# Kernel tuning notes

Measured on AMD Instinct MI355X. Metric: run time of the kernel, lower is better.

The kernel has to match this reference:

```python
import jax, jax.numpy as jnp
import numpy as np
import math

B, T, C, H = 2, 1024, 768, 12
HD = C // H


def _heads(t):
    # [B,T,C] -> [B,H,T,HD]
    return t.reshape(B, T, H, HD).transpose(0, 2, 1, 3)


def _causal_sdpa(q, k, v):
    # q,k,v: [B,H,T,HD]; scaled dot-product attention with causal mask, no dropout
    scale = 1.0 / math.sqrt(HD)
    s = jnp.einsum('bhqd,bhkd->bhqk', q, k) * scale
    mask = jnp.tril(jnp.ones((T, T), dtype=bool))
    s = jnp.where(mask, s, jnp.finfo(s.dtype).min)
    p = jax.nn.softmax(s, axis=-1)
    return jnp.einsum('bhqk,bhkd->bhqd', p, v)


def setup_inputs() -> dict:
    key = jax.random.key(0)
    k1, k2, k3 = jax.random.split(key, 3)
    x = jax.random.normal(k1, (B, T, C), dtype=jnp.float32)
    eps = 0.1
    x_lower = x - eps
    x_upper = x + eps
    W_attn = jax.random.normal(k2, (3 * C, C), dtype=jnp.float32) * 0.02
    W_proj = jax.random.normal(k3, (C, C), dtype=jnp.float32) * 0.02
    return {'x': x, 'x_lower': x_lower, 'x_upper': x_upper,
            'W_attn': W_attn, 'W_proj': W_proj}


def reference(x, x_lower, x_upper, W_attn, W_proj):
    # main path
    qkv = x @ W_attn.T                       # [B,T,3C]
    q, k, v = jnp.split(qkv, 3, axis=2)
    y = _causal_sdpa(_heads(q), _heads(k), _heads(v))
    y = y.transpose(0, 2, 1, 3).reshape(B, T, C) @ W_proj.T

    # interval bound path (torch runs it under no_grad)
    W_pos = jnp.maximum(W_attn, 0.0)
    W_neg = jnp.minimum(W_attn, 0.0)
    lowers = x_lower @ W_pos.T + x_upper @ W_neg.T   # lower bounds of q,k,v concat
    uppers = x_upper @ W_pos.T + x_lower @ W_neg.T   # upper bounds of q,k,v concat
    qL, kL, vL = (_heads(t) for t in jnp.split(lowers, 3, axis=2))
    qU, kU, vU = (_heads(t) for t in jnp.split(uppers, 3, axis=2))

    y_min = None
    y_max = None
    for qq in (qL, qU):
        for kk in (kL, kU):
            for vv in (vL, vU):
                yb = _causal_sdpa(qq, kk, vv)
                y_min = yb if y_min is None else jnp.minimum(y_min, yb)
                y_max = yb if y_max is None else jnp.maximum(y_max, yb)
    y_lower = y_min.transpose(0, 2, 1, 3).reshape(B, T, C) @ W_proj.T
    y_upper = y_max.transpose(0, 2, 1, 3).reshape(B, T, C) @ W_proj.T
    return (y, y_lower, y_upper)
```

## Files before the change

kernel.cpp:

```cpp
#include <hip/hip_runtime.h>
#include <stdint.h>
#include <math.h>

typedef __attribute__((ext_vector_type(8))) short bf16x8;
typedef __attribute__((ext_vector_type(4))) short s16x4;
typedef __attribute__((ext_vector_type(8))) short s16x8;
typedef __attribute__((ext_vector_type(4))) float f32x4;
typedef __attribute__((ext_vector_type(2))) uint32_t u32x2;

#define DEVI __device__ __forceinline__

constexpr int Bn = 2, Tn = 1024, Cn = 768, Hn = 12, HDn = 64;
constexpr int N3 = 3 * Cn;
constexpr int Mrows = Bn * Tn;
constexpr size_t SZy = (size_t)Mrows * Cn;

template <int V> struct IntC { static constexpr int value = V; };

DEVI short f2bf(float f) {
  union { float f; uint32_t u; } v; v.f = f;
  uint32_t u = v.u;
  return (short)((u + 0x7FFFu + ((u >> 16) & 1u)) >> 16);
}
DEVI float bf2f(short b) {
  union { uint32_t u; float f; } v; v.u = ((uint32_t)(uint16_t)b) << 16;
  return v.f;
}
DEVI float fexp2(float x) { return __builtin_exp2f(x); }
DEVI uint32_t cvtpk(float lo, float hi) {
  uint32_t r;
  asm("v_cvt_pk_bf16_f32 %0, %1, %2" : "=v"(r) : "v"(lo), "v"(hi));
  return r;
}
DEVI void cp16(void* lds, const void* g) {
  __builtin_amdgcn_global_load_lds(
      (const __attribute__((address_space(1))) uint32_t*)(uintptr_t)g,
      (__attribute__((address_space(3))) uint32_t*)(uint32_t)(uintptr_t)lds,
      16, 0, 0);
}
DEVI f32x4 fz() { f32x4 z; z[0] = 0.f; z[1] = 0.f; z[2] = 0.f; z[3] = 0.f; return z; }

__global__ void prep_x(const float* __restrict__ x, const float* __restrict__ xl,
                       const float* __restrict__ xu, short* __restrict__ xb,
                       short* __restrict__ mb, short* __restrict__ rb) {
  int i = blockIdx.x * 256 + threadIdx.x;
  float4 vx = ((const float4*)x)[i];
  float4 vl = ((const float4*)xl)[i];
  float4 vu = ((const float4*)xu)[i];
  s16x4 a, m_, g;
  a[0] = f2bf(vx.x); a[1] = f2bf(vx.y); a[2] = f2bf(vx.z); a[3] = f2bf(vx.w);
  m_[0] = f2bf(0.5f * (vl.x + vu.x)); m_[1] = f2bf(0.5f * (vl.y + vu.y));
  m_[2] = f2bf(0.5f * (vl.z + vu.z)); m_[3] = f2bf(0.5f * (vl.w + vu.w));
  g[0] = f2bf(0.5f * (vu.x - vl.x)); g[1] = f2bf(0.5f * (vu.y - vl.y));
  g[2] = f2bf(0.5f * (vu.z - vl.z)); g[3] = f2bf(0.5f * (vu.w - vl.w));
  ((s16x4*)xb)[i] = a; ((s16x4*)mb)[i] = m_; ((s16x4*)rb)[i] = g;
}
__global__ void prep_w(const float* __restrict__ w, short* __restrict__ wb,
                       short* __restrict__ awb) {
  int i = blockIdx.x * 256 + threadIdx.x;
  float4 v = ((const float4*)w)[i];
  s16x4 a, b2;
  a[0] = f2bf(v.x); a[1] = f2bf(v.y); a[2] = f2bf(v.z); a[3] = f2bf(v.w);
  b2[0] = f2bf(fabsf(v.x)); b2[1] = f2bf(fabsf(v.y));
  b2[2] = f2bf(fabsf(v.z)); b2[3] = f2bf(fabsf(v.w));
  ((s16x4*)wb)[i] = a; ((s16x4*)awb)[i] = b2;
}
__global__ void prep_w1(const float* __restrict__ w, short* __restrict__ wb) {
  int i = blockIdx.x * 256 + threadIdx.x;
  float4 v = ((const float4*)w)[i];
  s16x4 a;
  a[0] = f2bf(v.x); a[1] = f2bf(v.y); a[2] = f2bf(v.z); a[3] = f2bf(v.w);
  ((s16x4*)wb)[i] = a;
}

__launch_bounds__(256, 3)
__global__ void gemm_qkv3(const short* __restrict__ A0, const short* __restrict__ A1,
                          const short* __restrict__ A2, const short* __restrict__ B0,
                          const short* __restrict__ B1, short* __restrict__ qkv,
                          short* __restrict__ low, short* __restrict__ up) {
  constexpr int BM = 64, BN = 128;
  __shared__ short At[3 * BM * 32];
  __shared__ short Bt[2 * BN * 32];
  const int tid = threadIdx.x, wave = tid >> 6, lane = tid & 63;
  const int g = lane >> 4, q = lane & 15;
  const int wm = wave >> 1, wn = wave & 1;
  const int brow = blockIdx.x * BM, bcol = blockIdx.y * BN;
  const short* As[3] = {A0, A1, A2};
  const short* Bs[2] = {B0, B1};

  f32x4 acc[3][2][4];
#pragma unroll
  for (int a = 0; a < 3; a++)
#pragma unroll
    for (int m = 0; m < 2; m++)
#pragma unroll
      for (int n = 0; n < 4; n++) acc[a][m][n] = fz();

  const int arow = tid >> 2, ac = tid & 3;
  for (int kt = 0; kt < Cn / 32; ++kt) {
#pragma unroll
    for (int a = 0; a < 3; a++)
      cp16((char*)At + a * 4096 + tid * 16,
           As[a] + (size_t)(brow + arow) * Cn + (kt * 32 + ac * 8));
#pragma unroll
    for (int b2 = 0; b2 < 2; b2++)
#pragma unroll
      for (int ii = 0; ii < 2; ++ii) {
        int i = wave * 2 + ii;
        int ch = i * 64 + lane, row = ch >> 2, c = ch & 3;
        cp16((char*)Bt + b2 * 8192 + i * 1024,
             Bs[b2] + (size_t)(bcol + row) * Cn + (kt * 32 + c * 8));
      }
    __syncthreads();
    bf16x8 bfr[2][4];
#pragma unroll
    for (int b2 = 0; b2 < 2; b2++)
#pragma unroll
      for (int n = 0; n < 4; n++) {
        int r = wn * 64 + n * 16 + q;
        bfr[b2][n] = *(const bf16x8*)&Bt[b2 * (BN * 32) + r * 32 + g * 8];
      }
#pragma unroll
    for (int a = 0; a < 3; a++) {
      bf16x8 af[2];
#pragma unroll
      for (int m = 0; m < 2; m++) {
        int r = wm * 32 + m * 16 + q;
        af[m] = *(const bf16x8*)&At[a * (BM * 32) + r * 32 + g * 8];
      }
      const int bs = (a == 2) ? 1 : 0;
#pragma unroll
      for (int m = 0; m < 2; m++)
#pragma unroll
        for (int n = 0; n < 4; n++)
          acc[a][m][n] = __builtin_amdgcn_mfma_f32_16x16x32_bf16(
              af[m], bfr[bs][n], acc[a][m][n], 0, 0, 0);
    }
    __syncthreads();
  }
#pragma unroll
  for (int m = 0; m < 2; m++)
#pragma unroll
    for (int n = 0; n < 4; n++)
#pragma unroll
      for (int r = 0; r < 4; r++) {
        int row = brow + wm * 32 + m * 16 + g * 4 + r;
        int col = bcol + wn * 64 + n * 16 + q;
        size_t idx = (size_t)row * N3 + col;
        float v0 = acc[0][m][n][r], v1 = acc[1][m][n][r], v2 = acc[2][m][n][r];
        qkv[idx] = f2bf(v0);
        low[idx] = f2bf(v1 - v2);
        up[idx]  = f2bf(v1 + v2);
      }
}

__launch_bounds__(256, 4)
__global__ void gemm_proj(const short* __restrict__ A0, const short* __restrict__ A1,
                          const short* __restrict__ A2, const short* __restrict__ Bw,
                          float* __restrict__ out) {
  constexpr int BM = 64, BN = 128;
  __shared__ short At[BM * 32];
  __shared__ short Bt[BN * 32];
  const short* Ap = blockIdx.z == 0 ? A0 : (blockIdx.z == 1 ? A1 : A2);
  float* op = out + (size_t)blockIdx.z * SZy;
  const int tid = threadIdx.x, wave = tid >> 6, lane = tid & 63;
  const int wm = wave >> 1, wn = wave & 1;
  const int brow = blockIdx.x * BM, bcol = blockIdx.y * BN;

  f32x4 acc[2][4];
#pragma unroll
  for (int m = 0; m < 2; m++)
#pragma unroll
    for (int n = 0; n < 4; n++) acc[m][n] = fz();

  const int chunk = wave * 64 + lane, srow = chunk >> 2, sc = chunk & 3;
  for (int kt = 0; kt < Cn / 32; ++kt) {
    cp16((char*)At + wave * 1024, Ap + (size_t)(brow + srow) * Cn + (kt * 32 + sc * 8));
#pragma unroll
    for (int ii = 0; ii < 2; ++ii) {
      int i = wave * 2 + ii;
      int ch = i * 64 + lane, row = ch >> 2, c = ch & 3;
      cp16((char*)Bt + i * 1024, Bw + (size_t)(bcol + row) * Cn + (kt * 32 + c * 8));
    }
    __syncthreads();
    bf16x8 af[2], bfr[4];
#pragma unroll
    for (int m = 0; m < 2; m++) {
      int r = wm * 32 + m * 16 + (lane & 15);
      af[m] = *(const bf16x8*)&At[r * 32 + (lane >> 4) * 8];
    }
#pragma unroll
    for (int n = 0; n < 4; n++) {
      int r = wn * 64 + n * 16 + (lane & 15);
      bfr[n] = *(const bf16x8*)&Bt[r * 32 + (lane >> 4) * 8];
    }
#pragma unroll
    for (int m = 0; m < 2; m++)
#pragma unroll
      for (int n = 0; n < 4; n++)
        acc[m][n] = __builtin_amdgcn_mfma_f32_16x16x32_bf16(af[m], bfr[n], acc[m][n], 0, 0, 0);
    __syncthreads();
  }
#pragma unroll
  for (int m = 0; m < 2; m++)
#pragma unroll
    for (int n = 0; n < 4; n++)
#pragma unroll
      for (int r = 0; r < 4; r++) {
        int row = brow + wm * 32 + m * 16 + (lane >> 4) * 4 + r;
        int col = bcol + wn * 64 + n * 16 + (lane & 15);
        op[(size_t)row * Cn + col] = acc[m][n][r];
      }
}

__global__ void vtrans(const short* __restrict__ s0, const short* __restrict__ s1,
                       const short* __restrict__ s2, short* __restrict__ d0,
                       short* __restrict__ d1, short* __restrict__ d2) {
  __shared__ short tile[64][72];
  const short* src = blockIdx.z == 0 ? s0 : (blockIdx.z == 1 ? s1 : s2);
  short* dst = blockIdx.z == 0 ? d0 : (blockIdx.z == 1 ? d1 : d2);
  const int tt = blockIdx.x, bh = blockIdx.y;
  const int b = bh / Hn, h = bh % Hn;
  const int tid = threadIdx.x;
#pragma unroll
  for (int i = 0; i < 2; i++) {
    int chunk = i * 256 + tid;
    int t = chunk >> 3, c = chunk & 7;
    s16x8 v = *(const s16x8*)(src + (size_t)(b * Tn + tt * 64 + t) * N3 +
                              2 * Cn + h * HDn + c * 8);
    *(s16x8*)&tile[t][c * 8] = v;
  }
  __syncthreads();
#pragma unroll
  for (int i = 0; i < 2; i++) {
    int chunk = i * 256 + tid;
    int d = chunk >> 3, tc = chunk & 7;
    s16x8 v;
#pragma unroll
    for (int j = 0; j < 8; j++) v[j] = tile[tc * 8 + j][d];
    *(s16x8*)(dst + (size_t)bh * (64 * 1024) + (size_t)d * 1024 + tt * 64 + tc * 8) = v;
  }
}

__launch_bounds__(256, 3)
__global__ void flash_all(const short* __restrict__ qkv, const short* __restrict__ lowb,
                          const short* __restrict__ upb, const short* __restrict__ vtq,
                          const short* __restrict__ vtl, const short* __restrict__ vtu,
                          short* __restrict__ yab, short* __restrict__ comb) {
  constexpr float SCL = 0.18033688f;
  constexpr float THR = 8.0f / SCL;
  __shared__ short Kt[64 * 64];
  __shared__ short Vt0[64 * 64];
  __shared__ short Vt1[64 * 64];
  __shared__ short Pt[8 * 16 * 64];
  const int tid = threadIdx.x, wave = tid >> 6, lane = tid & 63;
  const int g = lane >> 4, q = lane & 15;
  const int bh = blockIdx.x, combo = blockIdx.y;
  const int j = 7 - blockIdx.z;
  const int qt0 = j * 128;
  const int b = bh / Hn, h = bh % Hn;
  const bool isMain = (combo == 4);
  const short* Qsrc = isMain ? qkv : ((combo & 2) ? upb : lowb);
  const short* Ksrc = isMain ? qkv : ((combo & 1) ? upb : lowb);
  const short* V0t = isMain ? vtq : vtl;
  const short* V1t = vtu;
  const int qswz = (q & 7) << 4;

  int koff[2], voff[2];
#pragma unroll
  for (int ii = 0; ii < 2; ++ii) {
    int chunk = (wave * 2 + ii) * 64 + lane, row = chunk >> 3, c = chunk & 7;
    int cg = c ^ (row & 7);
    koff[ii] = row * N3 + cg * 8;
    voff[ii] = row * 1024 + cg * 8;
  }
  const short* Kbase = Ksrc + (size_t)(b * Tn) * N3 + Cn + h * HDn;
  const short* V0base = V0t + (size_t)bh * (64 * 1024);
  const short* V1base = V1t + (size_t)bh * (64 * 1024);

  bf16x8 aq[2][2];
#pragma unroll
  for (int u = 0; u < 2; u++) {
    int trow = qt0 + u * 64 + wave * 16 + q;
    const short* qp = Qsrc + (size_t)(b * Tn + trow) * N3 + h * HDn;
#pragma unroll
    for (int s = 0; s < 2; s++) aq[u][s] = *(const bf16x8*)(qp + s * 32 + g * 8);
  }

  f32x4 o0[2][4], o1[2][4];
  float mrow[2], lrow[2];
#pragma unroll
  for (int u = 0; u < 2; u++) {
    mrow[u] = -INFINITY; lrow[u] = 0.f;
#pragma unroll
    for (int n = 0; n < 4; n++) { o0[u][n] = fz(); o1[u][n] = fz(); }
  }

  auto softmax_u = [&](f32x4 (&sv)[4], int u, auto diagc) {
    constexpr bool DIAG = decltype(diagc)::value;
    if constexpr (DIAG) {
      const int rhs = wave * 16 + q, kb = g * 4;
#pragma unroll
      for (int m = 0; m < 4; m++)
#pragma unroll
        for (int r = 0; r < 4; r++)
          sv[m][r] = (m * 16 + kb + r <= rhs) ? sv[m][r] : -INFINITY;
    }
    float mx = -INFINITY;
#pragma unroll
    for (int m = 0; m < 4; m++)
#pragma unroll
      for (int r = 0; r < 4; r++) mx = fmaxf(mx, sv[m][r]);
    mx = fmaxf(mx, __shfl_xor(mx, 16));
    mx = fmaxf(mx, __shfl_xor(mx, 32));
    if (!__all(mx <= mrow[u] + THR)) {
      float mnew = fmaxf(mrow[u], mx);
      float corr = fexp2((mrow[u] - mnew) * SCL);
      mrow[u] = mnew; lrow[u] *= corr;
#pragma unroll
      for (int n = 0; n < 4; n++) {
        o0[u][n][0] *= corr; o0[u][n][1] *= corr;
        o0[u][n][2] *= corr; o0[u][n][3] *= corr;
      }
      if (!isMain) {
#pragma unroll
        for (int n = 0; n < 4; n++) {
          o1[u][n][0] *= corr; o1[u][n][1] *= corr;
          o1[u][n][2] *= corr; o1[u][n][3] *= corr;
        }
      }
    }
    const float nms = -mrow[u] * SCL;
    float ps = 0.f;
#pragma unroll
    for (int m = 0; m < 4; m++)
#pragma unroll
      for (int r = 0; r < 4; r++) {
        float p = fexp2(fmaf(sv[m][r], SCL, nms));
        sv[m][r] = p;
        ps += p;
      }
    ps += __shfl_xor(ps, 16);
    ps += __shfl_xor(ps, 32);
    lrow[u] += ps;
    char* PtW = (char*)Pt + (wave * 2 + u) * 2048;
#pragma unroll
    for (int m = 0; m < 4; m++) {
      u32x2 w;
      w[0] = cvtpk(sv[m][0], sv[m][1]);
      w[1] = cvtpk(sv[m][2], sv[m][3]);
      *(u32x2*)(PtW + ((q * 128 + m * 32 + g * 8) ^ qswz)) = w;
    }
  };

  auto kv_iter = [&](int kv, auto m0c, auto m1c) {
    constexpr int M0 = decltype(m0c)::value;
    constexpr int M1 = decltype(m1c)::value;
#pragma unroll
    for (int ii = 0; ii < 2; ++ii)
      cp16((char*)Kt + (wave * 2 + ii) * 1024, Kbase + (size_t)kv * (64 * N3) + koff[ii]);
#pragma unroll
    for (int ii = 0; ii < 2; ++ii)
      cp16((char*)Vt0 + (wave * 2 + ii) * 1024, V0base + kv * 64 + voff[ii]);
    if (!isMain) {
#pragma unroll
      for (int ii = 0; ii < 2; ++ii)
        cp16((char*)Vt1 + (wave * 2 + ii) * 1024, V1base + kv * 64 + voff[ii]);
    }
    __syncthreads();

    f32x4 sa0[4], sa1[4];
#pragma unroll
    for (int m = 0; m < 4; m++) { sa0[m] = fz(); sa1[m] = fz(); }
    __builtin_amdgcn_s_setprio(1);
#pragma unroll
    for (int m = 0; m < 4; m++) {
#pragma unroll
      for (int s = 0; s < 2; s++) {
        int krow = m * 16 + q;
        bf16x8 bk = *(const bf16x8*)((char*)Kt +
            krow * 128 + ((g * 16 + s * 64) ^ ((krow & 7) << 4)));
        if constexpr (M0 > 0)
          sa0[m] = __builtin_amdgcn_mfma_f32_16x16x32_bf16(bk, aq[0][s], sa0[m], 0, 0, 0);
        if constexpr (M1 > 0)
          sa1[m] = __builtin_amdgcn_mfma_f32_16x16x32_bf16(bk, aq[1][s], sa1[m], 0, 0, 0);
      }
    }
    __builtin_amdgcn_s_setprio(0);

    if constexpr (M0 > 0) softmax_u(sa0, 0, IntC<(M0 == 1)>{});
    if constexpr (M1 > 0) softmax_u(sa1, 1, IntC<(M1 == 1)>{});

    __builtin_amdgcn_s_setprio(1);
#pragma unroll
    for (int kk = 0; kk < 2; kk++) {
      bf16x8 pb0, pb1;
      if constexpr (M0 > 0)
        pb0 = *(const bf16x8*)((char*)Pt + (wave * 2 + 0) * 2048 +
                               ((q * 128 + kk * 64 + g * 16) ^ qswz));
      if constexpr (M1 > 0)
        pb1 = *(const bf16x8*)((char*)Pt + (wave * 2 + 1) * 2048 +
                               ((q * 128 + kk * 64 + g * 16) ^ qswz));
#pragma unroll
      for (int mf = 0; mf < 4; mf++) {
        int drow = mf * 16 + q;
        int boff = drow * 128 + ((g * 16 + kk * 64) ^ ((drow & 7) << 4));
        bf16x8 av0 = *(const bf16x8*)((char*)Vt0 + boff);
        if constexpr (M0 > 0)
          o0[0][mf] = __builtin_amdgcn_mfma_f32_16x16x32_bf16(av0, pb0, o0[0][mf], 0, 0, 0);
        if constexpr (M1 > 0)
          o0[1][mf] = __builtin_amdgcn_mfma_f32_16x16x32_bf16(av0, pb1, o0[1][mf], 0, 0, 0);
        if (!isMain) {
          bf16x8 av1 = *(const bf16x8*)((char*)Vt1 + boff);
          if constexpr (M0 > 0)
            o1[0][mf] = __builtin_amdgcn_mfma_f32_16x16x32_bf16(av1, pb0, o1[0][mf], 0, 0, 0);
          if constexpr (M1 > 0)
            o1[1][mf] = __builtin_amdgcn_mfma_f32_16x16x32_bf16(av1, pb1, o1[1][mf], 0, 0, 0);
        }
      }
    }
    __builtin_amdgcn_s_setprio(0);
    __syncthreads();
  };

  const int jj = 2 * j;
  for (int kv = 0; kv < jj; ++kv) kv_iter(kv, IntC<2>{}, IntC<2>{});
  kv_iter(jj, IntC<1>{}, IntC<2>{});
  kv_iter(jj + 1, IntC<0>{}, IntC<1>{});

#pragma unroll
  for (int u = 0; u < 2; u++) {
    const float inv = 1.0f / lrow[u];
    const int trow = qt0 + u * 64 + wave * 16 + q;
    const size_t rowbase = (size_t)(b * Tn + trow) * Cn + h * HDn + g * 4;
#pragma unroll
    for (int mf = 0; mf < 4; mf++) {
      size_t idx = rowbase + mf * 16;
      u32x2 v0;
      v0[0] = cvtpk(o0[u][mf][0] * inv, o0[u][mf][1] * inv);
      v0[1] = cvtpk(o0[u][mf][2] * inv, o0[u][mf][3] * inv);
      if (isMain) {
        *(u32x2*)(yab + idx) = v0;
      } else {
        u32x2 v1;
        v1[0] = cvtpk(o1[u][mf][0] * inv, o1[u][mf][1] * inv);
        v1[1] = cvtpk(o1[u][mf][2] * inv, o1[u][mf][3] * inv);
        *(u32x2*)(comb + (size_t)(2 * combo) * SZy + idx) = v0;
        *(u32x2*)(comb + (size_t)(2 * combo + 1) * SZy + idx) = v1;
      }
    }
  }
}

__global__ void reduce_minmax(const short* __restrict__ comb, short* __restrict__ ymn,
                              short* __restrict__ ymx) {
  int i = blockIdx.x * 256 + threadIdx.x;
  s16x8 mn8 = ((const s16x8*)(comb + 0 * SZy))[i];
  s16x8 mx8 = ((const s16x8*)(comb + 1 * SZy))[i];
#pragma unroll
  for (int c = 1; c < 4; c++) {
    s16x8 a = ((const s16x8*)(comb + (size_t)(2 * c) * SZy))[i];
    s16x8 b2 = ((const s16x8*)(comb + (size_t)(2 * c + 1) * SZy))[i];
#pragma unroll
    for (int j = 0; j < 8; j++) {
      mn8[j] = f2bf(fminf(bf2f(mn8[j]), bf2f(a[j])));
      mx8[j] = f2bf(fmaxf(bf2f(mx8[j]), bf2f(b2[j])));
    }
  }
  ((s16x8*)ymn)[i] = mn8;
  ((s16x8*)ymx)[i] = mx8;
}

extern "C" void kernel_launch(void* const* d_in, const int* in_sizes, int n_in,
                              void* d_out, int out_size, void* d_ws, size_t ws_size,
                              hipStream_t stream) {
  const float* x  = (const float*)d_in[0];
  const float* xl = (const float*)d_in[1];
  const float* xu = (const float*)d_in[2];
  const float* Wa = (const float*)d_in[3];
  const float* Wp = (const float*)d_in[4];
  float* out = (float*)d_out;

  char* p = (char*)d_ws;
  auto carve = [&](size_t bytes) -> char* {
    char* r = p; p += (bytes + 255) & ~(size_t)255; return r;
  };
  short* xb   = (short*)carve((size_t)Mrows * Cn * 2);
  short* midb = (short*)carve((size_t)Mrows * Cn * 2);
  short* radb = (short*)carve((size_t)Mrows * Cn * 2);
  short* wb   = (short*)carve((size_t)N3 * Cn * 2);
  short* awb  = (short*)carve((size_t)N3 * Cn * 2);
  short* wpb  = (short*)carve((size_t)Cn * Cn * 2);
  short* qkvb = (short*)carve((size_t)Mrows * N3 * 2);
  short* lowb = (short*)carve((size_t)Mrows * N3 * 2);
  short* upb  = (short*)carve((size_t)Mrows * N3 * 2);
  short* vtq  = (short*)carve((size_t)24 * 64 * 1024 * 2);
  short* vtl  = (short*)carve((size_t)24 * 64 * 1024 * 2);
  short* vtu  = (short*)carve((size_t)24 * 64 * 1024 * 2);
  short* yab  = (short*)carve(SZy * 2);
  short* ymnb = (short*)carve(SZy * 2);
  short* ymxb = (short*)carve(SZy * 2);
  short* comb = (short*)carve(8 * SZy * 2);

  prep_x<<<1536, 256, 0, stream>>>(x, xl, xu, xb, midb, radb);
  prep_w<<<1728, 256, 0, stream>>>(Wa, wb, awb);
  prep_w1<<<576, 256, 0, stream>>>(Wp, wpb);

  gemm_qkv3<<<dim3(32, 18), 256, 0, stream>>>(xb, midb, radb, wb, awb,
                                              qkvb, lowb, upb);

  vtrans<<<dim3(16, 24, 3), 256, 0, stream>>>(qkvb, lowb, upb, vtq, vtl, vtu);

  flash_all<<<dim3(24, 5, 8), 256, 0, stream>>>(qkvb, lowb, upb, vtq, vtl, vtu,
                                                yab, comb);

  reduce_minmax<<<768, 256, 0, stream>>>(comb, ymnb, ymxb);

  gemm_proj<<<dim3(32, 6, 3), 256, 0, stream>>>(yab, ymnb, ymxb, wpb, out);
}
```

Baseline: 132.3 us.

## Double-buffer LDS tiles in GEMMs and attention K loads with explicit waitcnt barriers

Both GEMM kernels now keep two LDS buffers per operand and prefetch the next k-tile while MFMAs run on the current one. Each iteration ends with an explicit vmcnt/lgkmcnt wait plus a barrier instead of two __syncthreads. The attention kernel double-buffers K and prefetches the next KV block's K during the current iteration, using a partial vmcnt(2) wait before the PV stage. MFMA blocks get raised s_setprio, and gemm_qkv3 launch bounds drop from 3 to 2 waves per SIMD to fit the larger LDS footprint, which may cut occupancy. A stray extra LDS read (a comma expression reading At[0][0]) was left in the qkv B-fragment load, and the vmcnt(2) count depends on how many loads are outstanding in the isMain path.

```diff
diff --git a/kernel.cpp b/kernel.cpp
--- a/kernel.cpp
+++ b/kernel.cpp
@@ -39,6 +39,14 @@
       16, 0, 0);
 }
 DEVI f32x4 fz() { f32x4 z; z[0] = 0.f; z[1] = 0.f; z[2] = 0.f; z[3] = 0.f; return z; }
+DEVI void wait_vm2() {
+  asm volatile("s_waitcnt vmcnt(2)" ::: "memory");
+  __builtin_amdgcn_sched_barrier(0);
+}
+DEVI void wait_all() {
+  asm volatile("s_waitcnt vmcnt(0) lgkmcnt(0)" ::: "memory");
+  __builtin_amdgcn_sched_barrier(0);
+}
 
 __global__ void prep_x(const float* __restrict__ x, const float* __restrict__ xl,
                        const float* __restrict__ xu, short* __restrict__ xb,
@@ -73,14 +81,14 @@
   ((s16x4*)wb)[i] = a;
 }
 
-__launch_bounds__(256, 3)
+__launch_bounds__(256, 2)
 __global__ void gemm_qkv3(const short* __restrict__ A0, const short* __restrict__ A1,
                           const short* __restrict__ A2, const short* __restrict__ B0,
                           const short* __restrict__ B1, short* __restrict__ qkv,
                           short* __restrict__ low, short* __restrict__ up) {
   constexpr int BM = 64, BN = 128;
-  __shared__ short At[3 * BM * 32];
-  __shared__ short Bt[2 * BN * 32];
+  __shared__ short At[2][3 * BM * 32];
+  __shared__ short Bt[2][2 * BN * 32];
   const int tid = threadIdx.x, wave = tid >> 6, lane = tid & 63;
   const int g = lane >> 4, q = lane & 15;
   const int wm = wave >> 1, wn = wave & 1;
@@ -97,10 +105,10 @@
       for (int n = 0; n < 4; n++) acc[a][m][n] = fz();
 
   const int arow = tid >> 2, ac = tid & 3;
-  for (int kt = 0; kt < Cn / 32; ++kt) {
+  auto stage = [&](int kt, int p) {
 #pragma unroll
     for (int a = 0; a < 3; a++)
-      cp16((char*)At + a * 4096 + tid * 16,
+      cp16((char*)At[p] + a * 4096 + tid * 16,
            As[a] + (size_t)(brow + arow) * Cn + (kt * 32 + ac * 8));
 #pragma unroll
     for (int b2 = 0; b2 < 2; b2++)
@@ -108,17 +116,28 @@
       for (int ii = 0; ii < 2; ++ii) {
         int i = wave * 2 + ii;
         int ch = i * 64 + lane, row = ch >> 2, c = ch & 3;
-        cp16((char*)Bt + b2 * 8192 + i * 1024,
+        cp16((char*)Bt[p] + b2 * 8192 + i * 1024,
              Bs[b2] + (size_t)(bcol + row) * Cn + (kt * 32 + c * 8));
       }
-    __syncthreads();
+  };
+
+  stage(0, 0);
+  wait_all();
+  __builtin_amdgcn_s_barrier();
+
+  constexpr int NKT = Cn / 32;
+  for (int kt = 0; kt < NKT; ++kt) {
+    const int p = kt & 1;
+    stage(kt + 1 < NKT ? kt + 1 : kt, p ^ 1);
+    __builtin_amdgcn_sched_barrier(0);
     bf16x8 bfr[2][4];
 #pragma unroll
     for (int b2 = 0; b2 < 2; b2++)
 #pragma unroll
       for (int n = 0; n < 4; n++) {
         int r = wn * 64 + n * 16 + q;
-        bfr[b2][n] = *(const bf16x8*)&Bt[b2 * (BN * 32) + r * 32 + g * 8];
+        bfr[b2][n] = *(const bf16x8*)&At[0][0 ] ,
+        bfr[b2][n] = *(const bf16x8*)&Bt[p][b2 * (BN * 32) + r * 32 + g * 8];
       }
 #pragma unroll
     for (int a = 0; a < 3; a++) {
@@ -126,17 +145,20 @@
 #pragma unroll
       for (int m = 0; m < 2; m++) {
         int r = wm * 32 + m * 16 + q;
-        af[m] = *(const bf16x8*)&At[a * (BM * 32) + r * 32 + g * 8];
+        af[m] = *(const bf16x8*)&At[p][a * (BM * 32) + r * 32 + g * 8];
       }
       const int bs = (a == 2) ? 1 : 0;
+      __builtin_amdgcn_s_setprio(1);
 #pragma unroll
       for (int m = 0; m < 2; m++)
 #pragma unroll
         for (int n = 0; n < 4; n++)
           acc[a][m][n] = __builtin_amdgcn_mfma_f32_16x16x32_bf16(
               af[m], bfr[bs][n], acc[a][m][n], 0, 0, 0);
-    }
-    __syncthreads();
+      __builtin_amdgcn_s_setprio(0);
+    }
+    wait_all();
+    __builtin_amdgcn_s_barrier();
   }
 #pragma unroll
   for (int m = 0; m < 2; m++)
@@ -159,8 +181,8 @@
                           const short* __restrict__ A2, const short* __restrict__ Bw,
                           float* __restrict__ out) {
   constexpr int BM = 64, BN = 128;
-  __shared__ short At[BM * 32];
-  __shared__ short Bt[BN * 32];
+  __shared__ short At[2][BM * 32];
+  __shared__ short Bt[2][BN * 32];
   const short* Ap = blockIdx.z == 0 ? A0 : (blockIdx.z == 1 ? A1 : A2);
   float* op = out + (size_t)blockIdx.z * SZy;
   const int tid = threadIdx.x, wave = tid >> 6, lane = tid & 63;
@@ -173,33 +195,46 @@
 #pragma unroll
     for (int n = 0; n < 4; n++) acc[m][n] = fz();
 
-  const int chunk = wave * 64 + lane, srow = chunk >> 2, sc = chunk & 3;
-  for (int kt = 0; kt < Cn / 32; ++kt) {
-    cp16((char*)At + wave * 1024, Ap + (size_t)(brow + srow) * Cn + (kt * 32 + sc * 8));
+  const int arow = tid >> 2, ac = tid & 3;
+  auto stage = [&](int kt, int p) {
+    cp16((char*)At[p] + tid * 16, Ap + (size_t)(brow + arow) * Cn + (kt * 32 + ac * 8));
 #pragma unroll
     for (int ii = 0; ii < 2; ++ii) {
       int i = wave * 2 + ii;
       int ch = i * 64 + lane, row = ch >> 2, c = ch & 3;
-      cp16((char*)Bt + i * 1024, Bw + (size_t)(bcol + row) * Cn + (kt * 32 + c * 8));
-    }
-    __syncthreads();
+      cp16((char*)Bt[p] + i * 1024, Bw + (size_t)(bcol + row) * Cn + (kt * 32 + c * 8));
+    }
+  };
+
+  stage(0, 0);
+  wait_all();
+  __builtin_amdgcn_s_barrier();
+
+  constexpr int NKT = Cn / 32;
+  for (int kt = 0; kt < NKT; ++kt) {
+    const int p = kt & 1;
+    stage(kt + 1 < NKT ? kt + 1 : kt, p ^ 1);
+    __builtin_amdgcn_sched_barrier(0);
     bf16x8 af[2], bfr[4];
 #pragma unroll
     for (int m = 0; m < 2; m++) {
       int r = wm * 32 + m * 16 + (lane & 15);
-      af[m] = *(const bf16x8*)&At[r * 32 + (lane >> 4) * 8];
+      af[m] = *(const bf16x8*)&At[p][r * 32 + (lane >> 4) * 8];
     }
 #pragma unroll
     for (int n = 0; n < 4; n++) {
       int r = wn * 64 + n * 16 + (lane & 15);
-      bfr[n] = *(const bf16x8*)&Bt[r * 32 + (lane >> 4) * 8];
-    }
+      bfr[n] = *(const bf16x8*)&Bt[p][r * 32 + (lane >> 4) * 8];
+    }
+    __builtin_amdgcn_s_setprio(1);
 #pragma unroll
     for (int m = 0; m < 2; m++)
 #pragma unroll
       for (int n = 0; n < 4; n++)
         acc[m][n] = __builtin_amdgcn_mfma_f32_16x16x32_bf16(af[m], bfr[n], acc[m][n], 0, 0, 0);
-    __syncthreads();
+    __builtin_amdgcn_s_setprio(0);
+    wait_all();
+    __builtin_amdgcn_s_barrier();
   }
 #pragma unroll
   for (int m = 0; m < 2; m++)
@@ -249,7 +284,7 @@
                           short* __restrict__ yab, short* __restrict__ comb) {
   constexpr float SCL = 0.18033688f;
   constexpr float THR = 8.0f / SCL;
-  __shared__ short Kt[64 * 64];
+  __shared__ short Kt[2][64 * 64];
   __shared__ short Vt0[64 * 64];
   __shared__ short Vt1[64 * 64];
   __shared__ short Pt[8 * 16 * 64];
@@ -265,6 +300,7 @@
   const short* V0t = isMain ? vtq : vtl;
   const short* V1t = vtu;
   const int qswz = (q & 7) << 4;
+  const int jjmax = 2 * j + 1;
 
   int koff[2], voff[2];
 #pragma unroll
@@ -353,12 +389,15 @@
     }
   };
 
-  auto kv_iter = [&](int kv, auto m0c, auto m1c) {
+#pragma unroll
+  for (int ii = 0; ii < 2; ++ii)
+    cp16((char*)Kt[0] + (wave * 2 + ii) * 1024, Kbase + koff[ii]);
+  wait_all();
+  __builtin_amdgcn_s_barrier();
+
+  auto kv_iter = [&](int kv, int p, auto m0c, auto m1c) {
     constexpr int M0 = decltype(m0c)::value;
     constexpr int M1 = decltype(m1c)::value;
-#pragma unroll
-    for (int ii = 0; ii < 2; ++ii)
-      cp16((char*)Kt + (wave * 2 + ii) * 1024, Kbase + (size_t)kv * (64 * N3) + koff[ii]);
 #pragma unroll
     for (int ii = 0; ii < 2; ++ii)
       cp16((char*)Vt0 + (wave * 2 + ii) * 1024, V0base + kv * 64 + voff[ii]);
@@ -367,7 +406,15 @@
       for (int ii = 0; ii < 2; ++ii)
         cp16((char*)Vt1 + (wave * 2 + ii) * 1024, V1base + kv * 64 + voff[ii]);
     }
-    __syncthreads();
+    __builtin_amdgcn_sched_barrier(0);
+    {
+      int kvn = kv + 1 > jjmax ? jjmax : kv + 1;
+#pragma unroll
+      for (int ii = 0; ii < 2; ++ii)
+        cp16((char*)Kt[p ^ 1] + (wave * 2 + ii) * 1024,
+             Kbase + (size_t)kvn * (64 * N3) + koff[ii]);
+    }
+    __builtin_amdgcn_sched_barrier(0);
 
     f32x4 sa0[4], sa1[4];
 #pragma unroll
@@ -378,7 +425,7 @@
 #pragma unroll
       for (int s = 0; s < 2; s++) {
         int krow = m * 16 + q;
-        bf16x8 bk = *(const bf16x8*)((char*)Kt +
+        bf16x8 bk = *(const bf16x8*)((char*)Kt[p] +
             krow * 128 + ((g * 16 + s * 64) ^ ((krow & 7) << 4)));
         if constexpr (M0 > 0)
           sa0[m] = __builtin_amdgcn_mfma_f32_16x16x32_bf16(bk, aq[0][s], sa0[m], 0, 0, 0);
@@ -390,6 +437,9 @@
 
     if constexpr (M0 > 0) softmax_u(sa0, 0, IntC<(M0 == 1)>{});
     if constexpr (M1 > 0) softmax_u(sa1, 1, IntC<(M1 == 1)>{});
+
+    wait_vm2();
+    __builtin_amdgcn_s_barrier();
 
     __builtin_amdgcn_s_setprio(1);
 #pragma unroll
@@ -420,13 +470,15 @@
       }
     }
     __builtin_amdgcn_s_setprio(0);
-    __syncthreads();
+    wait_all();
+    __builtin_amdgcn_s_barrier();
   };
 
   const int jj = 2 * j;
-  for (int kv = 0; kv < jj; ++kv) kv_iter(kv, IntC<2>{}, IntC<2>{});
-  kv_iter(jj, IntC<1>{}, IntC<2>{});
-  kv_iter(jj + 1, IntC<0>{}, IntC<1>{});
+  int p = 0;
+  for (int kv = 0; kv < jj; ++kv) { kv_iter(kv, p, IntC<2>{}, IntC<2>{}); p ^= 1; }
+  kv_iter(jj, p, IntC<1>{}, IntC<2>{}); p ^= 1;
+  kv_iter(jj + 1, p, IntC<0>{}, IntC<1>{});
 
 #pragma unroll
   for (int u = 0; u < 2; u++) {
```

Result: slower. 136.6 us (+3.3%).

## Share K tiles across qL/qU combos and pair causal query tiles per block

Applied to the files above, without the earlier changes.

Restructures the flash attention grid so each block handles one K source (lower, upper or main) and computes both Q-lower and Q-upper against it. Each K/V tile is then loaded once and reused for two query variants, and the grid shrinks from 5 to 3 combos. Each block now processes a pair of 64-row query tiles (zp and 15-zp) in sequence, which balances causal work across blocks. It also swaps __syncthreads for an explicit waitcnt plus s_barrier. The cost is more accumulator registers per wave (four output sets), which may lower occupancy under the 3-block launch bound.

```diff
diff --git a/kernel.cpp b/kernel.cpp
--- a/kernel.cpp
+++ b/kernel.cpp
@@ -39,6 +39,10 @@
       16, 0, 0);
 }
 DEVI f32x4 fz() { f32x4 z; z[0] = 0.f; z[1] = 0.f; z[2] = 0.f; z[3] = 0.f; return z; }
+DEVI void wait_all() {
+  asm volatile("s_waitcnt vmcnt(0) lgkmcnt(0)" ::: "memory");
+  __builtin_amdgcn_sched_barrier(0);
+}
 
 __global__ void prep_x(const float* __restrict__ x, const float* __restrict__ xl,
                        const float* __restrict__ xu, short* __restrict__ xb,
@@ -252,18 +256,14 @@
   __shared__ short Kt[64 * 64];
   __shared__ short Vt0[64 * 64];
   __shared__ short Vt1[64 * 64];
-  __shared__ short Pt[8 * 16 * 64];
+  __shared__ short Pt[4 * 2 * 16 * 64];
   const int tid = threadIdx.x, wave = tid >> 6, lane = tid & 63;
   const int g = lane >> 4, q = lane & 15;
-  const int bh = blockIdx.x, combo = blockIdx.y;
-  const int j = 7 - blockIdx.z;
-  const int qt0 = j * 128;
+  const int bh = blockIdx.x, cz = blockIdx.y, zp = blockIdx.z;
   const int b = bh / Hn, h = bh % Hn;
-  const bool isMain = (combo == 4);
-  const short* Qsrc = isMain ? qkv : ((combo & 2) ? upb : lowb);
-  const short* Ksrc = isMain ? qkv : ((combo & 1) ? upb : lowb);
+  const bool isMain = (cz == 2);
+  const short* Ksrc = isMain ? qkv : (cz ? upb : lowb);
   const short* V0t = isMain ? vtq : vtl;
-  const short* V1t = vtu;
   const int qswz = (q & 7) << 4;
 
   int koff[2], voff[2];
@@ -276,27 +276,12 @@
   }
   const short* Kbase = Ksrc + (size_t)(b * Tn) * N3 + Cn + h * HDn;
   const short* V0base = V0t + (size_t)bh * (64 * 1024);
-  const short* V1base = V1t + (size_t)bh * (64 * 1024);
-
-  bf16x8 aq[2][2];
-#pragma unroll
-  for (int u = 0; u < 2; u++) {
-    int trow = qt0 + u * 64 + wave * 16 + q;
-    const short* qp = Qsrc + (size_t)(b * Tn + trow) * N3 + h * HDn;
-#pragma unroll
-    for (int s = 0; s < 2; s++) aq[u][s] = *(const bf16x8*)(qp + s * 32 + g * 8);
-  }
-
-  f32x4 o0[2][4], o1[2][4];
-  float mrow[2], lrow[2];
-#pragma unroll
-  for (int u = 0; u < 2; u++) {
-    mrow[u] = -INFINITY; lrow[u] = 0.f;
-#pragma unroll
-    for (int n = 0; n < 4; n++) { o0[u][n] = fz(); o1[u][n] = fz(); }
-  }
-
-  auto softmax_u = [&](f32x4 (&sv)[4], int u, auto diagc) {
+  const short* V1base = vtu + (size_t)bh * (64 * 1024);
+  char* PtL = (char*)Pt + (wave * 2 + 0) * 2048;
+  char* PtU = (char*)Pt + (wave * 2 + 1) * 2048;
+
+  auto softmax_v = [&](f32x4 (&sv)[4], float& m_, float& l_, f32x4 (&oA)[4],
+                       f32x4 (&oB)[4], bool hasB, char* PtW, auto diagc) {
     constexpr bool DIAG = decltype(diagc)::value;
     if constexpr (DIAG) {
       const int rhs = wave * 16 + q, kb = g * 4;
@@ -313,24 +298,22 @@
       for (int r = 0; r < 4; r++) mx = fmaxf(mx, sv[m][r]);
     mx = fmaxf(mx, __shfl_xor(mx, 16));
     mx = fmaxf(mx, __shfl_xor(mx, 32));
-    if (!__all(mx <= mrow[u] + THR)) {
-      float mnew = fmaxf(mrow[u], mx);
-      float corr = fexp2((mrow[u] - mnew) * SCL);
-      mrow[u] = mnew; lrow[u] *= corr;
+    if (!__all(mx <= m_ + THR)) {
+      float mnew = fmaxf(m_, mx);
+      float corr = fexp2((m_ - mnew) * SCL);
+      m_ = mnew; l_ *= corr;
 #pragma unroll
       for (int n = 0; n < 4; n++) {
-        o0[u][n][0] *= corr; o0[u][n][1] *= corr;
-        o0[u][n][2] *= corr; o0[u][n][3] *= corr;
-      }
-      if (!isMain) {
+        oA[n][0] *= corr; oA[n][1] *= corr; oA[n][2] *= corr; oA[n][3] *= corr;
+      }
+      if (hasB) {
 #pragma unroll
         for (int n = 0; n < 4; n++) {
-          o1[u][n][0] *= corr; o1[u][n][1] *= corr;
-          o1[u][n][2] *= corr; o1[u][n][3] *= corr;
+          oB[n][0] *= corr; oB[n][1] *= corr; oB[n][2] *= corr; oB[n][3] *= corr;
         }
       }
     }
-    const float nms = -mrow[u] * SCL;
+    const float nms = -m_ * SCL;
     float ps = 0.f;
 #pragma unroll
     for (int m = 0; m < 4; m++)
@@ -342,8 +325,7 @@
       }
     ps += __shfl_xor(ps, 16);
     ps += __shfl_xor(ps, 32);
-    lrow[u] += ps;
-    char* PtW = (char*)Pt + (wave * 2 + u) * 2048;
+    l_ += ps;
 #pragma unroll
     for (int m = 0; m < 4; m++) {
       u32x2 w;
@@ -353,100 +335,122 @@
     }
   };
 
-  auto kv_iter = [&](int kv, auto m0c, auto m1c) {
-    constexpr int M0 = decltype(m0c)::value;
-    constexpr int M1 = decltype(m1c)::value;
-#pragma unroll
-    for (int ii = 0; ii < 2; ++ii)
-      cp16((char*)Kt + (wave * 2 + ii) * 1024, Kbase + (size_t)kv * (64 * N3) + koff[ii]);
-#pragma unroll
-    for (int ii = 0; ii < 2; ++ii)
-      cp16((char*)Vt0 + (wave * 2 + ii) * 1024, V0base + kv * 64 + voff[ii]);
-    if (!isMain) {
+#pragma unroll
+  for (int ph = 0; ph < 2; ++ph) {
+    const int qt = ph ? (15 - zp) : zp;
+    const int trow = qt * 64 + wave * 16 + q;
+
+    bf16x8 aqL[2], aqU[2];
+    {
+      const short* qpL = (isMain ? qkv : lowb) + (size_t)(b * Tn + trow) * N3 + h * HDn;
+#pragma unroll
+      for (int s = 0; s < 2; s++) aqL[s] = *(const bf16x8*)(qpL + s * 32 + g * 8);
+      if (!isMain) {
+        const short* qpU = upb + (size_t)(b * Tn + trow) * N3 + h * HDn;
+#pragma unroll
+        for (int s = 0; s < 2; s++) aqU[s] = *(const bf16x8*)(qpU + s * 32 + g * 8);
+      }
+    }
+
+    f32x4 oL0[4], oL1[4], oU0[4], oU1[4];
+    float mL = -INFINITY, lL = 0.f, mU = -INFINITY, lU = 0.f;
+#pragma unroll
+    for (int n = 0; n < 4; n++) { oL0[n] = fz(); oL1[n] = fz(); oU0[n] = fz(); oU1[n] = fz(); }
+
+    auto kv_iter = [&](int kv, auto diagc) {
+      constexpr bool DIAG = decltype(diagc)::value;
 #pragma unroll
       for (int ii = 0; ii < 2; ++ii)
-        cp16((char*)Vt1 + (wave * 2 + ii) * 1024, V1base + kv * 64 + voff[ii]);
-    }
-    __syncthreads();
-
-    f32x4 sa0[4], sa1[4];
-#pragma unroll
-    for (int m = 0; m < 4; m++) { sa0[m] = fz(); sa1[m] = fz(); }
-    __builtin_amdgcn_s_setprio(1);
-#pragma unroll
-    for (int m = 0; m < 4; m++) {
-#pragma unroll
-      for (int s = 0; s < 2; s++) {
-        int krow = m * 16 + q;
-        bf16x8 bk = *(const bf16x8*)((char*)Kt +
-            krow * 128 + ((g * 16 + s * 64) ^ ((krow & 7) << 4)));
-        if constexpr (M0 > 0)
-          sa0[m] = __builtin_amdgcn_mfma_f32_16x16x32_bf16(bk, aq[0][s], sa0[m], 0, 0, 0);
-        if constexpr (M1 > 0)
-          sa1[m] = __builtin_amdgcn_mfma_f32_16x16x32_bf16(bk, aq[1][s], sa1[m], 0, 0, 0);
-      }
-    }
-    __builtin_amdgcn_s_setprio(0);
-
-    if constexpr (M0 > 0) softmax_u(sa0, 0, IntC<(M0 == 1)>{});
-    if constexpr (M1 > 0) softmax_u(sa1, 1, IntC<(M1 == 1)>{});
-
-    __builtin_amdgcn_s_setprio(1);
-#pragma unroll
-    for (int kk = 0; kk < 2; kk++) {
-      bf16x8 pb0, pb1;
-      if constexpr (M0 > 0)
-        pb0 = *(const bf16x8*)((char*)Pt + (wave * 2 + 0) * 2048 +
-                               ((q * 128 + kk * 64 + g * 16) ^ qswz));
-      if constexpr (M1 > 0)
-        pb1 = *(const bf16x8*)((char*)Pt + (wave * 2 + 1) * 2048 +
-                               ((q * 128 + kk * 64 + g * 16) ^ qswz));
+        cp16((char*)Kt + (wave * 2 + ii) * 1024, Kbase + (size_t)kv * (64 * N3) + koff[ii]);
+#pragma unroll
+      for (int ii = 0; ii < 2; ++ii)
+        cp16((char*)Vt0 + (wave * 2 + ii) * 1024, V0base + kv * 64 + voff[ii]);
+      if (!isMain) {
+#pragma unroll
+        for (int ii = 0; ii < 2; ++ii)
+          cp16((char*)Vt1 + (wave * 2 + ii) * 1024, V1base + kv * 64 + voff[ii]);
+      }
+      wait_all();
+      __builtin_amdgcn_s_barrier();
+
+      f32x4 saL[4], saU[4];
+#pragma unroll
+      for (int m = 0; m < 4; m++) { saL[m] = fz(); saU[m] = fz(); }
+      __builtin_amdgcn_s_setprio(1);
+#pragma unroll
+      for (int m = 0; m < 4; m++) {
+#pragma unroll
+        for (int s = 0; s < 2; s++) {
+          int krow = m * 16 + q;
+          bf16x8 bk = *(const bf16x8*)((char*)Kt +
+              krow * 128 + ((g * 16 + s * 64) ^ ((krow & 7) << 4)));
+          saL[m] = __builtin_amdgcn_mfma_f32_16x16x32_bf16(bk, aqL[s], saL[m], 0, 0, 0);
+          if (!isMain)
+            saU[m] = __builtin_amdgcn_mfma_f32_16x16x32_bf16(bk, aqU[s], saU[m], 0, 0, 0);
+        }
+      }
+      __builtin_amdgcn_s_setprio(0);
+
+      softmax_v(saL, mL, lL, oL0, oL1, !isMain, PtL, diagc);
+      if (!isMain) softmax_v(saU, mU, lU, oU0, oU1, true, PtU, diagc);
+
+      __builtin_amdgcn_s_setprio(1);
+#pragma unroll
+      for (int kk = 0; kk < 2; kk++) {
+        bf16x8 pbL = *(const bf16x8*)(PtL + ((q * 128 + kk * 64 + g * 16) ^ qswz));
+        bf16x8 pbU;
+        if (!isMain)
+          pbU = *(const bf16x8*)(PtU + ((q * 128 + kk * 64 + g * 16) ^ qswz));
+#pragma unroll
+        for (int mf = 0; mf < 4; mf++) {
+          int drow = mf * 16 + q;
+          int boff = drow * 128 + ((g * 16 + kk * 64) ^ ((drow & 7) << 4));
+          bf16x8 av0 = *(const bf16x8*)((char*)Vt0 + boff);
+          oL0[mf] = __builtin_amdgcn_mfma_f32_16x16x32_bf16(av0, pbL, oL0[mf], 0, 0, 0);
+          if (!isMain) {
+            oU0[mf] = __builtin_amdgcn_mfma_f32_16x16x32_bf16(av0, pbU, oU0[mf], 0, 0, 0);
+            bf16x8 av1 = *(const bf16x8*)((char*)Vt1 + boff);
+            oL1[mf] = __builtin_amdgcn_mfma_f32_16x16x32_bf16(av1, pbL, oL1[mf], 0, 0, 0);
+            oU1[mf] = __builtin_amdgcn_mfma_f32_16x16x32_bf16(av1, pbU, oU1[mf], 0, 0, 0);
+          }
+        }
+      }
+      __builtin_amdgcn_s_setprio(0);
+      __builtin_amdgcn_s_barrier();
+    };
+
+    for (int kv = 0; kv < qt; ++kv) kv_iter(kv, IntC<0>{});
+    kv_iter(qt, IntC<1>{});
+
+    const float invL = 1.0f / lL;
+    const size_t rowbase = (size_t)(b * Tn + trow) * Cn + h * HDn + g * 4;
+    if (isMain) {
 #pragma unroll
       for (int mf = 0; mf < 4; mf++) {
-        int drow = mf * 16 + q;
-        int boff = drow * 128 + ((g * 16 + kk * 64) ^ ((drow & 7) << 4));
-        bf16x8 av0 = *(const bf16x8*)((char*)Vt0 + boff);
-        if constexpr (M0 > 0)
-          o0[0][mf] = __builtin_amdgcn_mfma_f32_16x16x32_bf16(av0, pb0, o0[0][mf], 0, 0, 0);
-        if constexpr (M1 > 0)
-          o0[1][mf] = __builtin_amdgcn_mfma_f32_16x16x32_bf16(av0, pb1, o0[1][mf], 0, 0, 0);
-        if (!isMain) {
-          bf16x8 av1 = *(const bf16x8*)((char*)Vt1 + boff);
-          if constexpr (M0 > 0)
-            o1[0][mf] = __builtin_amdgcn_mfma_f32_16x16x32_bf16(av1, pb0, o1[0][mf], 0, 0, 0);
-          if constexpr (M1 > 0)
-            o1[1][mf] = __builtin_amdgcn_mfma_f32_16x16x32_bf16(av1, pb1, o1[1][mf], 0, 0, 0);
-        }
-      }
-    }
-    __builtin_amdgcn_s_setprio(0);
-    __syncthreads();
-  };
-
-  const int jj = 2 * j;
-  for (int kv = 0; kv < jj; ++kv) kv_iter(kv, IntC<2>{}, IntC<2>{});
-  kv_iter(jj, IntC<1>{}, IntC<2>{});
-  kv_iter(jj + 1, IntC<0>{}, IntC<1>{});
-
-#pragma unroll
-  for (int u = 0; u < 2; u++) {
-    const float inv = 1.0f / lrow[u];
-    const int trow = qt0 + u * 64 + wave * 16 + q;
-    const size_t rowbase = (size_t)(b * Tn + trow) * Cn + h * HDn + g * 4;
-#pragma unroll
-    for (int mf = 0; mf < 4; mf++) {
-      size_t idx = rowbase + mf * 16;
-      u32x2 v0;
-      v0[0] = cvtpk(o0[u][mf][0] * inv, o0[u][mf][1] * inv);
-      v0[1] = cvtpk(o0[u][mf][2] * inv, o0[u][mf][3] * inv);
-      if (isMain) {
-        *(u32x2*)(yab + idx) = v0;
-      } else {
-        u32x2 v1;
-        v1[0] = cvtpk(o1[u][mf][0] * inv, o1[u][mf][1] * inv);
-        v1[1] = cvtpk(o1[u][mf][2] * inv, o1[u][mf][3] * inv);
-        *(u32x2*)(comb + (size_t)(2 * combo) * SZy + idx) = v0;
-        *(u32x2*)(comb + (size_t)(2 * combo + 1) * SZy + idx) = v1;
+        u32x2 v0;
+        v0[0] = cvtpk(oL0[mf][0] * invL, oL0[mf][1] * invL);
+        v0[1] = cvtpk(oL0[mf][2] * invL, oL0[mf][3] * invL);
+        *(u32x2*)(yab + rowbase + mf * 16) = v0;
+      }
+    } else {
+      const float invU = 1.0f / lU;
+      const int cL = cz, cU = 2 + cz;
+#pragma unroll
+      for (int mf = 0; mf < 4; mf++) {
+        size_t idx = rowbase + mf * 16;
+        u32x2 a0, a1, b0, b1;
+        a0[0] = cvtpk(oL0[mf][0] * invL, oL0[mf][1] * invL);
+        a0[1] = cvtpk(oL0[mf][2] * invL, oL0[mf][3] * invL);
+        a1[0] = cvtpk(oL1[mf][0] * invL, oL1[mf][1] * invL);
+        a1[1] = cvtpk(oL1[mf][2] * invL, oL1[mf][3] * invL);
+        b0[0] = cvtpk(oU0[mf][0] * invU, oU0[mf][1] * invU);
+        b0[1] = cvtpk(oU0[mf][2] * invU, oU0[mf][3] * invU);
+        b1[0] = cvtpk(oU1[mf][0] * invU, oU1[mf][1] * invU);
+        b1[1] = cvtpk(oU1[mf][2] * invU, oU1[mf][3] * invU);
+        *(u32x2*)(comb + (size_t)(2 * cL) * SZy + idx)     = a0;
+        *(u32x2*)(comb + (size_t)(2 * cL + 1) * SZy + idx) = a1;
+        *(u32x2*)(comb + (size_t)(2 * cU) * SZy + idx)     = b0;
+        *(u32x2*)(comb + (size_t)(2 * cU + 1) * SZy + idx) = b1;
       }
     }
   }
@@ -511,7 +515,7 @@
 
   vtrans<<<dim3(16, 24, 3), 256, 0, stream>>>(qkvb, lowb, upb, vtq, vtl, vtu);
 
-  flash_all<<<dim3(24, 5, 8), 256, 0, stream>>>(qkvb, lowb, upb, vtq, vtl, vtu,
+  flash_all<<<dim3(24, 3, 8), 256, 0, stream>>>(qkvb, lowb, upb, vtq, vtl, vtu,
                                                 yab, comb);
 
   reduce_minmax<<<768, 256, 0, stream>>>(comb, ymnb, ymxb);
```

New measurement: 156.7 us. +18.5%, slower.
